# Kernel optimization log

Measured on AMD Instinct MI355X. Metric: run time of the kernel, lower is better.

The kernel has to match this reference:

```python
import jax, jax.numpy as jnp
import numpy as np


def _gcs_conv(x, a, w1, w2, b):
    # GCSConv: relu(A @ x W1 + x W2 + b);  x:[B,N,F], a:[B,N,N]
    return jax.nn.relu(jnp.einsum('bij,bjh->bih', a, x @ w1) + x @ w2 + b)


def _topk_pool(x, a, p, ratio=0.5):
    # score y = x . p/||p||, keep top ceil(ratio*N) nodes per graph,
    # gate kept node features with sigmoid(y), slice adjacency rows+cols.
    y = x @ (p / jnp.linalg.norm(p))            # [B, N]
    k = int(np.ceil(ratio * y.shape[1]))
    yk, idx = jax.lax.top_k(y, k)               # [B, k]
    xk = jnp.take_along_axis(x, idx[:, :, None], axis=1)
    xk = xk * jax.nn.sigmoid(yk)[:, :, None]    # gated node features [B,k,H]
    ak = jnp.take_along_axis(a, idx[:, :, None], axis=1)
    ak = jnp.take_along_axis(ak, idx[:, None, :], axis=2)  # [B,k,k]
    return xk, ak


def setup_inputs() -> dict:
    B, N, F0, H, C = 256, 512, 128, 32, 16
    key = jax.random.key(0)
    ks = jax.random.split(key, 12)
    s = lambda fan: 1.0 / np.sqrt(fan)
    return {
        'x': jax.random.normal(ks[0], (B, N, F0), jnp.float32),
        'a': jax.random.uniform(ks[1], (B, N, N), jnp.float32),
        'w1_1': jax.random.normal(ks[2], (F0, H), jnp.float32) * s(F0),
        'w2_1': jax.random.normal(ks[3], (F0, H), jnp.float32) * s(F0),
        'b1': jnp.zeros((H,), jnp.float32),
        'w1_2': jax.random.normal(ks[4], (H, H), jnp.float32) * s(H),
        'w2_2': jax.random.normal(ks[5], (H, H), jnp.float32) * s(H),
        'b2': jnp.zeros((H,), jnp.float32),
        'w1_3': jax.random.normal(ks[6], (H, H), jnp.float32) * s(H),
        'w2_3': jax.random.normal(ks[7], (H, H), jnp.float32) * s(H),
        'b3': jnp.zeros((H,), jnp.float32),
        'p_pool': jax.random.normal(ks[8], (H,), jnp.float32),
        'wd': jax.random.normal(ks[9], (H, C), jnp.float32) * s(H),
        'bd': jnp.zeros((C,), jnp.float32),
    }


def reference(x, a, w1_1, w2_1, b1, w1_2, w2_2, b2, w1_3, w2_3, b3, p_pool, wd, bd):
    x = _gcs_conv(x, a, w1_1, w2_1, b1)
    # NOTE: original code reuses pool1 twice -> shared p_pool for both stages
    x1, a1 = _topk_pool(x, a, p_pool)
    x1 = _gcs_conv(x1, a1, w1_2, w2_2, b2)
    x2, a2 = _topk_pool(x1, a1, p_pool)
    x2 = _gcs_conv(x2, a2, w1_3, w2_3, b3)
    pooled = jnp.mean(x2, axis=1)               # GlobalAvgPool over nodes [B,H]
    return jax.nn.softmax(pooled @ wd + bd, axis=-1)
```

## Files before the change

### kernel.cpp

```cpp
#include <hip/hip_runtime.h>
#include <cmath>

#define B 256
#define N0 512
#define F0 128
#define H 32
#define NC 16

typedef short v8s __attribute__((ext_vector_type(8)));
typedef float v4f __attribute__((ext_vector_type(4)));
typedef unsigned short v8u __attribute__((ext_vector_type(8)));

__device__ inline ushort bf16_rne(float f) {
  unsigned u = __float_as_uint(f);
  unsigned r = (u + 0x7FFF + ((u >> 16) & 1)) >> 16;
  return (ushort)r;
}
__device__ inline float bf16_f(ushort s) { return __uint_as_float((unsigned)s << 16); }

template<int F, int RPT>
__global__ __launch_bounds__(256) void k_xw1(
    const float* __restrict__ x, const float* __restrict__ w1,
    const float* __restrict__ w2, const float* __restrict__ bias,
    ushort* __restrict__ hTh, ushort* __restrict__ hTl, float* __restrict__ g) {
  __shared__ float w1t[H][F + 4];
  __shared__ float w2t[H][F + 4];
  __shared__ float bs[H];
  __shared__ __align__(16) ushort thi[H][72];
  __shared__ __align__(16) ushort tlo[H][72];
  const int tid = threadIdx.x;
  for (int i = tid; i < F * H; i += 256) {
    int f = i >> 5, hc = i & 31;
    w1t[hc][f] = w1[i];
    w2t[hc][f] = w2[i];
  }
  if (tid < H) bs[tid] = bias[tid];
  __syncthreads();
  const int hq = tid & 7;
  const int rq = tid >> 3;
  const size_t row0 = (size_t)blockIdx.x * (32 * RPT) + (size_t)rq * RPT;
  const float* xb = x + row0 * F;
  float acc1[RPT][4];
  float acc2[RPT][4];
  #pragma unroll
  for (int r = 0; r < RPT; ++r)
    for (int c = 0; c < 4; ++c) { acc1[r][c] = 0.f; acc2[r][c] = 0.f; }
  for (int f0 = 0; f0 < F; f0 += 4) {
    float4 w1v[4], w2v[4];
    #pragma unroll
    for (int hh = 0; hh < 4; ++hh) {
      w1v[hh] = *(const float4*)&w1t[hq * 4 + hh][f0];
      w2v[hh] = *(const float4*)&w2t[hq * 4 + hh][f0];
    }
    #pragma unroll
    for (int r = 0; r < RPT; ++r) {
      float4 xv = *(const float4*)(xb + (size_t)r * F + f0);
      #pragma unroll
      for (int hh = 0; hh < 4; ++hh) {
        acc1[r][hh] += xv.x * w1v[hh].x + xv.y * w1v[hh].y + xv.z * w1v[hh].z + xv.w * w1v[hh].w;
        acc2[r][hh] += xv.x * w2v[hh].x + xv.y * w2v[hh].y + xv.z * w2v[hh].z + xv.w * w2v[hh].w;
      }
    }
  }
  #pragma unroll
  for (int r = 0; r < RPT; ++r) {
    size_t o = (row0 + r) * H + hq * 4;
    *(float4*)(g + o) = make_float4(acc2[r][0] + bs[hq * 4 + 0], acc2[r][1] + bs[hq * 4 + 1],
                                    acc2[r][2] + bs[hq * 4 + 2], acc2[r][3] + bs[hq * 4 + 3]);
    #pragma unroll
    for (int c = 0; c < 4; ++c) {
      float v = acc1[r][c];
      ushort hi = bf16_rne(v);
      thi[hq * 4 + c][rq * RPT + r] = hi;
      tlo[hq * 4 + c][rq * RPT + r] = bf16_rne(v - bf16_f(hi));
    }
  }
  __syncthreads();
  const int b = blockIdx.x >> 3;
  const int j0 = (blockIdx.x & 7) * 64;
  const int hrow = tid >> 3, seg = tid & 7;
  size_t o = ((size_t)b * H + hrow) * N0 + j0 + seg * 8;
  *(uint4*)&hTh[o] = *(const uint4*)&thi[hrow][seg * 8];
  *(uint4*)&hTl[o] = *(const uint4*)&tlo[hrow][seg * 8];
}

template<int NPREV, int K, int RPT>
__global__ __launch_bounds__(256) void k_xwg(
    const float* __restrict__ xsrc, const int* __restrict__ lidx,
    const float* __restrict__ gate,
    const float* __restrict__ w1, const float* __restrict__ w2,
    const float* __restrict__ bias,
    float* __restrict__ h, float* __restrict__ g) {
  constexpr int F = H;
  __shared__ float w1t[H][F + 4];
  __shared__ float w2t[H][F + 4];
  __shared__ float bs[H];
  const int tid = threadIdx.x;
  for (int i = tid; i < F * H; i += 256) {
    int f = i >> 5, hc = i & 31;
    w1t[hc][f] = w1[i];
    w2t[hc][f] = w2[i];
  }
  if (tid < H) bs[tid] = bias[tid];
  __syncthreads();
  const int hq = tid & 7;
  const int rq = tid >> 3;
  const int row0 = blockIdx.x * (32 * RPT) + rq * RPT;
  const int b = row0 / K;
  const float* xg0 = xsrc + (size_t)b * NPREV * H;
  int li[RPT];
  float gt[RPT];
  #pragma unroll
  for (int r = 0; r < RPT; ++r) { li[r] = lidx[row0 + r]; gt[r] = gate[row0 + r]; }
  float acc1[RPT][4];
  float acc2[RPT][4];
  #pragma unroll
  for (int r = 0; r < RPT; ++r)
    for (int c = 0; c < 4; ++c) { acc1[r][c] = 0.f; acc2[r][c] = 0.f; }
  for (int f0 = 0; f0 < F; f0 += 4) {
    float4 w1v[4], w2v[4];
    #pragma unroll
    for (int hh = 0; hh < 4; ++hh) {
      w1v[hh] = *(const float4*)&w1t[hq * 4 + hh][f0];
      w2v[hh] = *(const float4*)&w2t[hq * 4 + hh][f0];
    }
    #pragma unroll
    for (int r = 0; r < RPT; ++r) {
      float4 xv = *(const float4*)(xg0 + (size_t)li[r] * H + f0);
      #pragma unroll
      for (int hh = 0; hh < 4; ++hh) {
        acc1[r][hh] += xv.x * w1v[hh].x + xv.y * w1v[hh].y + xv.z * w1v[hh].z + xv.w * w1v[hh].w;
        acc2[r][hh] += xv.x * w2v[hh].x + xv.y * w2v[hh].y + xv.z * w2v[hh].z + xv.w * w2v[hh].w;
      }
    }
  }
  #pragma unroll
  for (int r = 0; r < RPT; ++r) {
    size_t o = ((size_t)row0 + r) * H + hq * 4;
    *(float4*)(h + o) = make_float4(acc1[r][0] * gt[r], acc1[r][1] * gt[r],
                                    acc1[r][2] * gt[r], acc1[r][3] * gt[r]);
    *(float4*)(g + o) = make_float4(acc2[r][0] * gt[r] + bs[hq * 4 + 0],
                                    acc2[r][1] * gt[r] + bs[hq * 4 + 1],
                                    acc2[r][2] * gt[r] + bs[hq * 4 + 2],
                                    acc2[r][3] * gt[r] + bs[hq * 4 + 3]);
  }
}

template<int K>
__global__ __launch_bounds__(512) void k_trans_inv(
    const float* __restrict__ hd, const int* __restrict__ idx,
    ushort* __restrict__ hTh, ushort* __restrict__ hTl) {
  __shared__ float hs[K][33];
  __shared__ int inv[N0];
  const int tid = threadIdx.x;
  const int b = blockIdx.x;
  for (int j = tid; j < N0; j += 512) inv[j] = -1;
  __syncthreads();
  for (int k = tid; k < K; k += 512) inv[idx[(size_t)b * K + k]] = k;
  for (int t = tid; t < K * 8; t += 512) {
    int r = t >> 3, c4 = t & 7;
    float4 v = *(const float4*)(hd + (((size_t)b * K) + r) * H + c4 * 4);
    hs[r][c4 * 4 + 0] = v.x;
    hs[r][c4 * 4 + 1] = v.y;
    hs[r][c4 * 4 + 2] = v.z;
    hs[r][c4 * 4 + 3] = v.w;
  }
  __syncthreads();
  for (int t = tid; t < H * 64; t += 512) {
    int hr = t >> 6, seg = t & 63;
    v8u hv, lv;
    #pragma unroll
    for (int i = 0; i < 8; ++i) {
      int k = inv[seg * 8 + i];
      float v = (k >= 0) ? hs[k][hr] : 0.f;
      ushort hi = bf16_rne(v);
      hv[i] = hi;
      lv[i] = bf16_rne(v - bf16_f(hi));
    }
    size_t o = ((size_t)b * H + hr) * N0 + seg * 8;
    *(v8u*)&hTh[o] = hv;
    *(v8u*)&hTl[o] = lv;
  }
}

template<int NROW>
__global__ __launch_bounds__(256) void k_ammx(
    const float* __restrict__ a0, const int* __restrict__ rid,
    const ushort* __restrict__ hTh, const ushort* __restrict__ hTl,
    const float* __restrict__ g, const float* __restrict__ p,
    float* __restrict__ out, float* __restrict__ yout) {
  constexpr int RB = 64;
  constexpr int KC = 32;
  constexpr int ASP = KC + 8;
  __shared__ ushort ah[RB][ASP];
  __shared__ ushort al[RB][ASP];
  __shared__ ushort bh[H][ASP];
  __shared__ ushort bl[H][ASP];
  __shared__ int rowid[RB];
  __shared__ float psu[H];
  __shared__ float pns_s;
  const int tid = threadIdx.x;
  const int b = blockIdx.x;
  const int row0 = blockIdx.y * RB;
  if (tid < RB) rowid[tid] = rid ? rid[(size_t)b * NROW + row0 + tid] : row0 + tid;
  if (yout && tid == 0) {
    float s = 0.f;
    for (int i = 0; i < H; ++i) s += p[i] * p[i];
    pns_s = 1.f / sqrtf(s);
  }
  __syncthreads();
  if (yout && tid < H) psu[tid] = p[tid] * pns_s;
  const int wave = tid >> 6, lane = tid & 63;
  const int m = lane & 15, quad = lane >> 4;
  const int sr = tid >> 2, skq = tid & 3;
  const int shh = tid >> 3, sseg = tid & 7;
  const float* ap = a0 + (size_t)b * N0 * N0 + (size_t)rowid[sr] * N0 + skq * 4;
  const ushort* bhsrc = hTh + ((size_t)b * H + shh) * N0 + sseg * 4;
  const ushort* blsrc = hTl + ((size_t)b * H + shh) * N0 + sseg * 4;
  v4f acc0 = {0.f, 0.f, 0.f, 0.f};
  v4f acc1 = {0.f, 0.f, 0.f, 0.f};
  float4 pA0 = *(const float4*)(ap);
  float4 pA1 = *(const float4*)(ap + 16);
  ushort4 pBh = *(const ushort4*)(bhsrc);
  ushort4 pBl = *(const ushort4*)(blsrc);
  for (int k0 = 0; k0 < N0; k0 += KC) {
    float4 nA0, nA1;
    ushort4 nBh, nBl;
    if (k0 + KC < N0) {
      nA0 = *(const float4*)(ap + k0 + KC);
      nA1 = *(const float4*)(ap + k0 + KC + 16);
      nBh = *(const ushort4*)(bhsrc + k0 + KC);
      nBl = *(const ushort4*)(blsrc + k0 + KC);
    }
    if (k0) __syncthreads();
    {
      ushort4 h0, l0, h1, l1;
      h0.x = bf16_rne(pA0.x); l0.x = bf16_rne(pA0.x - bf16_f(h0.x));
      h0.y = bf16_rne(pA0.y); l0.y = bf16_rne(pA0.y - bf16_f(h0.y));
      h0.z = bf16_rne(pA0.z); l0.z = bf16_rne(pA0.z - bf16_f(h0.z));
      h0.w = bf16_rne(pA0.w); l0.w = bf16_rne(pA0.w - bf16_f(h0.w));
      h1.x = bf16_rne(pA1.x); l1.x = bf16_rne(pA1.x - bf16_f(h1.x));
      h1.y = bf16_rne(pA1.y); l1.y = bf16_rne(pA1.y - bf16_f(h1.y));
      h1.z = bf16_rne(pA1.z); l1.z = bf16_rne(pA1.z - bf16_f(h1.z));
      h1.w = bf16_rne(pA1.w); l1.w = bf16_rne(pA1.w - bf16_f(h1.w));
      *(ushort4*)&ah[sr][skq * 4] = h0;      *(ushort4*)&al[sr][skq * 4] = l0;
      *(ushort4*)&ah[sr][skq * 4 + 16] = h1; *(ushort4*)&al[sr][skq * 4 + 16] = l1;
    }
    *(ushort4*)&bh[shh][sseg * 4] = pBh;
    *(ushort4*)&bl[shh][sseg * 4] = pBl;
    __syncthreads();
    const int arow = wave * 16 + m;
    v8s Ah = *(const v8s*)&ah[arow][quad * 8];
    v8s Al = *(const v8s*)&al[arow][quad * 8];
    v8s Bh0 = *(const v8s*)&bh[m][quad * 8];
    v8s Bh1 = *(const v8s*)&bh[16 + m][quad * 8];
    v8s Bl0 = *(const v8s*)&bl[m][quad * 8];
    v8s Bl1 = *(const v8s*)&bl[16 + m][quad * 8];
    acc0 = __builtin_amdgcn_mfma_f32_16x16x32_bf16(Ah, Bh0, acc0, 0, 0, 0);
    acc1 = __builtin_amdgcn_mfma_f32_16x16x32_bf16(Ah, Bh1, acc1, 0, 0, 0);
    acc0 = __builtin_amdgcn_mfma_f32_16x16x32_bf16(Al, Bh0, acc0, 0, 0, 0);
    acc1 = __builtin_amdgcn_mfma_f32_16x16x32_bf16(Al, Bh1, acc1, 0, 0, 0);
    acc0 = __builtin_amdgcn_mfma_f32_16x16x32_bf16(Ah, Bl0, acc0, 0, 0, 0);
    acc1 = __builtin_amdgcn_mfma_f32_16x16x32_bf16(Ah, Bl1, acc1, 0, 0, 0);
    pA0 = nA0; pA1 = nA1; pBh = nBh; pBl = nBl;
  }
  float part[4];
  #pragma unroll
  for (int reg = 0; reg < 4; ++reg) {
    int row = row0 + wave * 16 + quad * 4 + reg;
    size_t o0 = ((size_t)b * NROW + row) * H + m;
    size_t o1 = o0 + 16;
    float v0 = fmaxf(acc0[reg] + g[o0], 0.f);
    float v1 = fmaxf(acc1[reg] + g[o1], 0.f);
    out[o0] = v0;
    out[o1] = v1;
    if (yout) part[reg] = v0 * psu[m] + v1 * psu[m + 16];
  }
  if (yout) {
    #pragma unroll
    for (int reg = 0; reg < 4; ++reg)
      #pragma unroll
      for (int off = 1; off < 16; off <<= 1)
        part[reg] += __shfl_xor(part[reg], off, 16);
    if (m < 4)
      yout[(size_t)b * NROW + row0 + wave * 16 + quad * 4 + m] = part[m];
  }
}

template<int NN, int K>
__global__ __launch_bounds__(256) void k_topk(
    const float* __restrict__ y, const int* __restrict__ prev_idx,
    int* __restrict__ lidx, float* __restrict__ gate, int* __restrict__ out_idx) {
  __shared__ float ys[NN];
  __shared__ int is[NN];
  const int tid = threadIdx.x;
  const int b = blockIdx.x;
  for (int i = tid; i < NN; i += 256) {
    ys[i] = y[(size_t)b * NN + i];
    is[i] = i;
  }
  for (int k = 2; k <= NN; k <<= 1) {
    for (int j = k >> 1; j > 0; j >>= 1) {
      __syncthreads();
      for (int i = tid; i < NN; i += 256) {
        int ixj = i ^ j;
        if (ixj > i) {
          float v0 = ys[i], v1 = ys[ixj];
          int i0 = is[i], i1 = is[ixj];
          bool pre = (v1 > v0) || (v1 == v0 && i1 < i0);
          bool doswap = ((i & k) == 0) ? pre : !pre;
          if (doswap) { ys[i] = v1; ys[ixj] = v0; is[i] = i1; is[ixj] = i0; }
        }
      }
    }
  }
  for (int k = 2; k <= K; k <<= 1) {
    for (int j = k >> 1; j > 0; j >>= 1) {
      __syncthreads();
      for (int i = tid; i < K; i += 256) {
        int ixj = i ^ j;
        if (ixj > i && ixj < K) {
          float v0 = ys[i], v1 = ys[ixj];
          int i0 = is[i], i1 = is[ixj];
          bool pre = (i1 < i0);
          bool doswap = ((i & k) == 0) ? pre : !pre;
          if (doswap) { ys[i] = v1; ys[ixj] = v0; is[i] = i1; is[ixj] = i0; }
        }
      }
    }
  }
  __syncthreads();
  for (int t = tid; t < K; t += 256) {
    lidx[(size_t)b * K + t] = is[t];
    gate[(size_t)b * K + t] = 1.f / (1.f + expf(-ys[t]));
    out_idx[(size_t)b * K + t] = prev_idx ? prev_idx[(size_t)b * NN + is[t]] : is[t];
  }
}

__global__ __launch_bounds__(128) void k_head(
    const float* __restrict__ xl3, const float* __restrict__ wd,
    const float* __restrict__ bd, float* __restrict__ out) {
  __shared__ float part[4][H];
  __shared__ float pooled[H];
  __shared__ float wds[H * NC];
  __shared__ float logits[NC];
  const int tid = threadIdx.x;
  const int b = blockIdx.x;
  for (int i = tid; i < H * NC; i += 128) wds[i] = wd[i];
  const int f = tid & 31, nq = tid >> 5;
  float s = 0.f;
  for (int n = nq * 32; n < nq * 32 + 32; ++n)
    s += xl3[((size_t)b * 128 + n) * H + f];
  part[nq][f] = s;
  __syncthreads();
  if (tid < H)
    pooled[tid] = (part[0][tid] + part[1][tid] + part[2][tid] + part[3][tid]) * (1.f / 128.f);
  __syncthreads();
  if (tid < NC) {
    float acc = bd[tid];
    for (int i = 0; i < H; ++i) acc += pooled[i] * wds[i * NC + tid];
    logits[tid] = acc;
  }
  __syncthreads();
  if (tid == 0) {
    float mx = logits[0];
    for (int i = 1; i < NC; ++i) mx = fmaxf(mx, logits[i]);
    float e[NC], se = 0.f;
    for (int i = 0; i < NC; ++i) { e[i] = expf(logits[i] - mx); se += e[i]; }
    float inv = 1.f / se;
    for (int i = 0; i < NC; ++i) out[(size_t)b * NC + i] = e[i] * inv;
  }
}

extern "C" void kernel_launch(void* const* d_in, const int* in_sizes, int n_in,
                              void* d_out, int out_size, void* d_ws, size_t ws_size,
                              hipStream_t stream) {
  (void)in_sizes; (void)n_in; (void)out_size; (void)ws_size;
  const float* x    = (const float*)d_in[0];
  const float* a    = (const float*)d_in[1];
  const float* w1_1 = (const float*)d_in[2];
  const float* w2_1 = (const float*)d_in[3];
  const float* b1   = (const float*)d_in[4];
  const float* w1_2 = (const float*)d_in[5];
  const float* w2_2 = (const float*)d_in[6];
  const float* b2   = (const float*)d_in[7];
  const float* w1_3 = (const float*)d_in[8];
  const float* w2_3 = (const float*)d_in[9];
  const float* b3   = (const float*)d_in[10];
  const float* pp   = (const float*)d_in[11];
  const float* wd   = (const float*)d_in[12];
  const float* bd   = (const float*)d_in[13];
  float* out = (float*)d_out;

  char* w = (char*)d_ws;
  auto take = [&](size_t bytes) { char* r = w; w += (bytes + 255) & ~(size_t)255; return r; };
  ushort* hTh = (ushort*)take((size_t)B * H * N0 * 2);
  ushort* hTl = (ushort*)take((size_t)B * H * N0 * 2);
  float*  g1  = (float*) take((size_t)B * N0 * H * 4);
  float*  xl1 = (float*) take((size_t)B * N0 * H * 4);
  float*  y1  = (float*) take((size_t)B * N0 * 4);
  int*    id1 = (int*)   take((size_t)B * 256 * 4);
  int*    li1 = (int*)   take((size_t)B * 256 * 4);
  float*  gt1 = (float*) take((size_t)B * 256 * 4);
  float*  h2  = (float*) take((size_t)B * 256 * H * 4);
  float*  g2  = (float*) take((size_t)B * 256 * H * 4);
  float*  xl2 = (float*) take((size_t)B * 256 * H * 4);
  float*  y2  = (float*) take((size_t)B * 256 * 4);
  int*    id2 = (int*)   take((size_t)B * 128 * 4);
  int*    li2 = (int*)   take((size_t)B * 128 * 4);
  float*  gt2 = (float*) take((size_t)B * 128 * 4);
  float*  h3  = (float*) take((size_t)B * 128 * H * 4);
  float*  g3  = (float*) take((size_t)B * 128 * H * 4);
  float*  xl3 = (float*) take((size_t)B * 128 * H * 4);

  k_xw1<F0, 2><<<dim3(B * N0 / 64), dim3(256), 0, stream>>>(x, w1_1, w2_1, b1, hTh, hTl, g1);
  k_ammx<512><<<dim3(B, 8), dim3(256), 0, stream>>>(a, nullptr, hTh, hTl, g1, pp, xl1, y1);
  k_topk<512, 256><<<dim3(B), dim3(256), 0, stream>>>(y1, nullptr, li1, gt1, id1);
  k_xwg<512, 256, 4><<<dim3(B * 256 / 128), dim3(256), 0, stream>>>(xl1, li1, gt1, w1_2, w2_2, b2, h2, g2);
  k_trans_inv<256><<<dim3(B), dim3(512), 0, stream>>>(h2, id1, hTh, hTl);
  k_ammx<256><<<dim3(B, 4), dim3(256), 0, stream>>>(a, id1, hTh, hTl, g2, pp, xl2, y2);
  k_topk<256, 128><<<dim3(B), dim3(256), 0, stream>>>(y2, id1, li2, gt2, id2);
  k_xwg<256, 128, 4><<<dim3(B * 128 / 128), dim3(256), 0, stream>>>(xl2, li2, gt2, w1_3, w2_3, b3, h3, g3);
  k_trans_inv<128><<<dim3(B), dim3(512), 0, stream>>>(h3, id2, hTh, hTl);
  k_ammx<128><<<dim3(B, 2), dim3(256), 0, stream>>>(a, id2, hTh, hTl, g3, nullptr, xl3, nullptr);
  k_head<<<dim3(B), dim3(128), 0, stream>>>(xl3, wd, bd, out);
}
```

Before: 581.0 us.

## Fuse top-k, gated feature transform and transpose into one per-graph kernel

Merges the top-k sort, the gathered x@W1/x@W2 projection with sigmoid gating, and the inverse-index bf16 hi/lo transpose into a single kernel with one block per graph. This removes two kernel launches per pooling stage and the global round trips for the lidx, gate and h intermediates, which now stay in shared memory. In exchange, the projection runs with only 256 blocks (one per graph) with a larger shared-memory footprint, which lowers occupancy compared with the separately gridded kernels.

```diff
diff --git a/kernel.cpp b/kernel.cpp
--- a/kernel.cpp
+++ b/kernel.cpp
@@ -84,18 +84,68 @@
   *(uint4*)&hTl[o] = *(const uint4*)&tlo[hrow][seg * 8];
 }
 
-template<int NPREV, int K, int RPT>
-__global__ __launch_bounds__(256) void k_xwg(
-    const float* __restrict__ xsrc, const int* __restrict__ lidx,
-    const float* __restrict__ gate,
+template<int NN, int K>
+__global__ __launch_bounds__(256) void k_pxt(
+    const float* __restrict__ y, const int* __restrict__ prev_idx,
+    const float* __restrict__ xsrc,
     const float* __restrict__ w1, const float* __restrict__ w2,
     const float* __restrict__ bias,
-    float* __restrict__ h, float* __restrict__ g) {
+    int* __restrict__ out_idx, float* __restrict__ g,
+    ushort* __restrict__ hTh, ushort* __restrict__ hTl) {
   constexpr int F = H;
+  __shared__ float ys[NN];
+  __shared__ int is[NN];
+  __shared__ int gix[K];
+  __shared__ float gts[K];
   __shared__ float w1t[H][F + 4];
   __shared__ float w2t[H][F + 4];
   __shared__ float bs[H];
+  __shared__ float hs[K][36];
+  __shared__ int inv[N0];
   const int tid = threadIdx.x;
+  const int b = blockIdx.x;
+  for (int i = tid; i < NN; i += 256) {
+    ys[i] = y[(size_t)b * NN + i];
+    is[i] = i;
+  }
+  for (int k = 2; k <= NN; k <<= 1) {
+    for (int j = k >> 1; j > 0; j >>= 1) {
+      __syncthreads();
+      for (int i = tid; i < NN; i += 256) {
+        int ixj = i ^ j;
+        if (ixj > i) {
+          float v0 = ys[i], v1 = ys[ixj];
+          int i0 = is[i], i1 = is[ixj];
+          bool pre = (v1 > v0) || (v1 == v0 && i1 < i0);
+          bool doswap = ((i & k) == 0) ? pre : !pre;
+          if (doswap) { ys[i] = v1; ys[ixj] = v0; is[i] = i1; is[ixj] = i0; }
+        }
+      }
+    }
+  }
+  for (int k = 2; k <= K; k <<= 1) {
+    for (int j = k >> 1; j > 0; j >>= 1) {
+      __syncthreads();
+      for (int i = tid; i < K; i += 256) {
+        int ixj = i ^ j;
+        if (ixj > i && ixj < K) {
+          float v0 = ys[i], v1 = ys[ixj];
+          int i0 = is[i], i1 = is[ixj];
+          bool pre = (i1 < i0);
+          bool doswap = ((i & k) == 0) ? pre : !pre;
+          if (doswap) { ys[i] = v1; ys[ixj] = v0; is[i] = i1; is[ixj] = i0; }
+        }
+      }
+    }
+  }
+  __syncthreads();
+  for (int t = tid; t < K; t += 256) {
+    int gi = prev_idx ? prev_idx[(size_t)b * NN + is[t]] : is[t];
+    gix[t] = gi;
+    gts[t] = 1.f / (1.f + expf(-ys[t]));
+    out_idx[(size_t)b * K + t] = gi;
+  }
+  for (int j = tid; j < N0; j += 256) inv[j] = -1;
   for (int i = tid; i < F * H; i += 256) {
     int f = i >> 5, hc = i & 31;
     w1t[hc][f] = w1[i];
@@ -103,76 +153,39 @@
   }
   if (tid < H) bs[tid] = bias[tid];
   __syncthreads();
+  for (int t = tid; t < K; t += 256) inv[gix[t]] = t;
   const int hq = tid & 7;
   const int rq = tid >> 3;
-  const int row0 = blockIdx.x * (32 * RPT) + rq * RPT;
-  const int b = row0 / K;
-  const float* xg0 = xsrc + (size_t)b * NPREV * H;
-  int li[RPT];
-  float gt[RPT];
-  #pragma unroll
-  for (int r = 0; r < RPT; ++r) { li[r] = lidx[row0 + r]; gt[r] = gate[row0 + r]; }
-  float acc1[RPT][4];
-  float acc2[RPT][4];
-  #pragma unroll
-  for (int r = 0; r < RPT; ++r)
-    for (int c = 0; c < 4; ++c) { acc1[r][c] = 0.f; acc2[r][c] = 0.f; }
-  for (int f0 = 0; f0 < F; f0 += 4) {
-    float4 w1v[4], w2v[4];
-    #pragma unroll
-    for (int hh = 0; hh < 4; ++hh) {
-      w1v[hh] = *(const float4*)&w1t[hq * 4 + hh][f0];
-      w2v[hh] = *(const float4*)&w2t[hq * 4 + hh][f0];
-    }
-    #pragma unroll
-    for (int r = 0; r < RPT; ++r) {
-      float4 xv = *(const float4*)(xg0 + (size_t)li[r] * H + f0);
+  const float* xg0 = xsrc + (size_t)b * NN * H;
+  for (int rc = 0; rc < K; rc += 32) {
+    const int row = rc + rq;
+    const int li = is[row];
+    const float gt = gts[row];
+    float a1[4] = {0.f, 0.f, 0.f, 0.f};
+    float a2[4] = {0.f, 0.f, 0.f, 0.f};
+    for (int f0 = 0; f0 < F; f0 += 4) {
+      float4 xv = *(const float4*)(xg0 + (size_t)li * H + f0);
       #pragma unroll
       for (int hh = 0; hh < 4; ++hh) {
-        acc1[r][hh] += xv.x * w1v[hh].x + xv.y * w1v[hh].y + xv.z * w1v[hh].z + xv.w * w1v[hh].w;
-        acc2[r][hh] += xv.x * w2v[hh].x + xv.y * w2v[hh].y + xv.z * w2v[hh].z + xv.w * w2v[hh].w;
+        float4 w1v = *(const float4*)&w1t[hq * 4 + hh][f0];
+        float4 w2v = *(const float4*)&w2t[hq * 4 + hh][f0];
+        a1[hh] += xv.x * w1v.x + xv.y * w1v.y + xv.z * w1v.z + xv.w * w1v.w;
+        a2[hh] += xv.x * w2v.x + xv.y * w2v.y + xv.z * w2v.z + xv.w * w2v.w;
       }
     }
-  }
-  #pragma unroll
-  for (int r = 0; r < RPT; ++r) {
-    size_t o = ((size_t)row0 + r) * H + hq * 4;
-    *(float4*)(h + o) = make_float4(acc1[r][0] * gt[r], acc1[r][1] * gt[r],
-                                    acc1[r][2] * gt[r], acc1[r][3] * gt[r]);
-    *(float4*)(g + o) = make_float4(acc2[r][0] * gt[r] + bs[hq * 4 + 0],
-                                    acc2[r][1] * gt[r] + bs[hq * 4 + 1],
-                                    acc2[r][2] * gt[r] + bs[hq * 4 + 2],
-                                    acc2[r][3] * gt[r] + bs[hq * 4 + 3]);
-  }
-}
-
-template<int K>
-__global__ __launch_bounds__(512) void k_trans_inv(
-    const float* __restrict__ hd, const int* __restrict__ idx,
-    ushort* __restrict__ hTh, ushort* __restrict__ hTl) {
-  __shared__ float hs[K][33];
-  __shared__ int inv[N0];
-  const int tid = threadIdx.x;
-  const int b = blockIdx.x;
-  for (int j = tid; j < N0; j += 512) inv[j] = -1;
-  __syncthreads();
-  for (int k = tid; k < K; k += 512) inv[idx[(size_t)b * K + k]] = k;
-  for (int t = tid; t < K * 8; t += 512) {
-    int r = t >> 3, c4 = t & 7;
-    float4 v = *(const float4*)(hd + (((size_t)b * K) + r) * H + c4 * 4);
-    hs[r][c4 * 4 + 0] = v.x;
-    hs[r][c4 * 4 + 1] = v.y;
-    hs[r][c4 * 4 + 2] = v.z;
-    hs[r][c4 * 4 + 3] = v.w;
-  }
-  __syncthreads();
-  for (int t = tid; t < H * 64; t += 512) {
+    size_t o = ((size_t)b * K + row) * H + hq * 4;
+    *(float4*)(g + o) = make_float4(a2[0] * gt + bs[hq * 4 + 0], a2[1] * gt + bs[hq * 4 + 1],
+                                    a2[2] * gt + bs[hq * 4 + 2], a2[3] * gt + bs[hq * 4 + 3]);
+    *(float4*)&hs[row][hq * 4] = make_float4(a1[0] * gt, a1[1] * gt, a1[2] * gt, a1[3] * gt);
+  }
+  __syncthreads();
+  for (int t = tid; t < H * 64; t += 256) {
     int hr = t >> 6, seg = t & 63;
     v8u hv, lv;
     #pragma unroll
     for (int i = 0; i < 8; ++i) {
-      int k = inv[seg * 8 + i];
-      float v = (k >= 0) ? hs[k][hr] : 0.f;
+      int kk = inv[seg * 8 + i];
+      float v = (kk >= 0) ? hs[kk][hr] : 0.f;
       ushort hi = bf16_rne(v);
       hv[i] = hi;
       lv[i] = bf16_rne(v - bf16_f(hi));
@@ -287,56 +300,6 @@
   }
 }
 
-template<int NN, int K>
-__global__ __launch_bounds__(256) void k_topk(
-    const float* __restrict__ y, const int* __restrict__ prev_idx,
-    int* __restrict__ lidx, float* __restrict__ gate, int* __restrict__ out_idx) {
-  __shared__ float ys[NN];
-  __shared__ int is[NN];
-  const int tid = threadIdx.x;
-  const int b = blockIdx.x;
-  for (int i = tid; i < NN; i += 256) {
-    ys[i] = y[(size_t)b * NN + i];
-    is[i] = i;
-  }
-  for (int k = 2; k <= NN; k <<= 1) {
-    for (int j = k >> 1; j > 0; j >>= 1) {
-      __syncthreads();
-      for (int i = tid; i < NN; i += 256) {
-        int ixj = i ^ j;
-        if (ixj > i) {
-          float v0 = ys[i], v1 = ys[ixj];
-          int i0 = is[i], i1 = is[ixj];
-          bool pre = (v1 > v0) || (v1 == v0 && i1 < i0);
-          bool doswap = ((i & k) == 0) ? pre : !pre;
-          if (doswap) { ys[i] = v1; ys[ixj] = v0; is[i] = i1; is[ixj] = i0; }
-        }
-      }
-    }
-  }
-  for (int k = 2; k <= K; k <<= 1) {
-    for (int j = k >> 1; j > 0; j >>= 1) {
-      __syncthreads();
-      for (int i = tid; i < K; i += 256) {
-        int ixj = i ^ j;
-        if (ixj > i && ixj < K) {
-          float v0 = ys[i], v1 = ys[ixj];
-          int i0 = is[i], i1 = is[ixj];
-          bool pre = (i1 < i0);
-          bool doswap = ((i & k) == 0) ? pre : !pre;
-          if (doswap) { ys[i] = v1; ys[ixj] = v0; is[i] = i1; is[ixj] = i0; }
-        }
-      }
-    }
-  }
-  __syncthreads();
-  for (int t = tid; t < K; t += 256) {
-    lidx[(size_t)b * K + t] = is[t];
-    gate[(size_t)b * K + t] = 1.f / (1.f + expf(-ys[t]));
-    out_idx[(size_t)b * K + t] = prev_idx ? prev_idx[(size_t)b * NN + is[t]] : is[t];
-  }
-}
-
 __global__ __launch_bounds__(128) void k_head(
     const float* __restrict__ xl3, const float* __restrict__ wd,
     const float* __restrict__ bd, float* __restrict__ out) {
@@ -400,28 +363,18 @@
   float*  xl1 = (float*) take((size_t)B * N0 * H * 4);
   float*  y1  = (float*) take((size_t)B * N0 * 4);
   int*    id1 = (int*)   take((size_t)B * 256 * 4);
-  int*    li1 = (int*)   take((size_t)B * 256 * 4);
-  float*  gt1 = (float*) take((size_t)B * 256 * 4);
-  float*  h2  = (float*) take((size_t)B * 256 * H * 4);
   float*  g2  = (float*) take((size_t)B * 256 * H * 4);
   float*  xl2 = (float*) take((size_t)B * 256 * H * 4);
   float*  y2  = (float*) take((size_t)B * 256 * 4);
   int*    id2 = (int*)   take((size_t)B * 128 * 4);
-  int*    li2 = (int*)   take((size_t)B * 128 * 4);
-  float*  gt2 = (float*) take((size_t)B * 128 * 4);
-  float*  h3  = (float*) take((size_t)B * 128 * H * 4);
   float*  g3  = (float*) take((size_t)B * 128 * H * 4);
   float*  xl3 = (float*) take((size_t)B * 128 * H * 4);
 
   k_xw1<F0, 2><<<dim3(B * N0 / 64), dim3(256), 0, stream>>>(x, w1_1, w2_1, b1, hTh, hTl, g1);
   k_ammx<512><<<dim3(B, 8), dim3(256), 0, stream>>>(a, nullptr, hTh, hTl, g1, pp, xl1, y1);
-  k_topk<512, 256><<<dim3(B), dim3(256), 0, stream>>>(y1, nullptr, li1, gt1, id1);
-  k_xwg<512, 256, 4><<<dim3(B * 256 / 128), dim3(256), 0, stream>>>(xl1, li1, gt1, w1_2, w2_2, b2, h2, g2);
-  k_trans_inv<256><<<dim3(B), dim3(512), 0, stream>>>(h2, id1, hTh, hTl);
+  k_pxt<512, 256><<<dim3(B), dim3(256), 0, stream>>>(y1, nullptr, xl1, w1_2, w2_2, b2, id1, g2, hTh, hTl);
   k_ammx<256><<<dim3(B, 4), dim3(256), 0, stream>>>(a, id1, hTh, hTl, g2, pp, xl2, y2);
-  k_topk<256, 128><<<dim3(B), dim3(256), 0, stream>>>(y2, id1, li2, gt2, id2);
-  k_xwg<256, 128, 4><<<dim3(B * 128 / 128), dim3(256), 0, stream>>>(xl2, li2, gt2, w1_3, w2_3, b3, h3, g3);
-  k_trans_inv<128><<<dim3(B), dim3(512), 0, stream>>>(h3, id2, hTh, hTl);
+  k_pxt<256, 128><<<dim3(B), dim3(256), 0, stream>>>(y2, id1, xl2, w1_3, w2_3, b3, id2, g3, hTh, hTl);
   k_ammx<128><<<dim3(B, 2), dim3(256), 0, stream>>>(a, id2, hTh, hTl, g3, nullptr, xl3, nullptr);
   k_head<<<dim3(B), dim3(128), 0, stream>>>(xl3, wd, bd, out);
 }
```

Result: slower. 628.2 us (+8.1%).
